# Kernel tuning notes

Measured on AMD Instinct MI355X. Metric: run time of the kernel, lower is better.

## Reference

```python
import jax, jax.numpy as jnp
import numpy as np

N, E, D = 50000, 800000, 128
H, C = 8, 16  # heads, hidden_per_head; H*C == D
NEG_SLOPE = 0.15


def setup_inputs() -> dict:
    key = jax.random.key(0)
    ks = jax.random.split(key, 8)
    x = jax.random.normal(ks[0], (N, D), dtype=jnp.float32)
    edge_index = jax.random.randint(ks[1], (2, E), 0, N, dtype=jnp.int32)
    s = 1.0 / np.sqrt(D)
    return {
        "x": x,
        "edge_index": edge_index,
        "ln_g": jnp.ones((D,), jnp.float32),
        "ln_b": jnp.zeros((D,), jnp.float32),
        "W_l": jax.random.normal(ks[2], (D, H * C), jnp.float32) * s,
        "b_l": jnp.zeros((H * C,), jnp.float32),
        "W_r": jax.random.normal(ks[3], (D, H * C), jnp.float32) * s,
        "b_r": jnp.zeros((H * C,), jnp.float32),
        "att": jax.random.normal(ks[4], (H, C), jnp.float32) * (1.0 / np.sqrt(C)),
        "bias": jnp.zeros((H * C,), jnp.float32),
    }


def _layernorm(x, g, b, eps=1e-5):
    mu = jnp.mean(x, axis=-1, keepdims=True)
    var = jnp.mean(jnp.square(x - mu), axis=-1, keepdims=True)
    return (x - mu) * jax.lax.rsqrt(var + eps) * g + b


def reference(x, edge_index, ln_g, ln_b, W_l, b_l, W_r, b_r, att, bias):
    src, dst = edge_index[0], edge_index[1]
    h = _layernorm(x, ln_g, ln_b)                      # [N, D]
    xl = (h @ W_l + b_l).reshape(N, H, C)              # source-side transform
    xr = (h @ W_r + b_r).reshape(N, H, C)              # target-side transform
    # GATv2 edge attention: leaky_relu(x_j + x_i) . att
    e = xl[src] + xr[dst]                              # [E, H, C]
    e_act = jnp.where(e > 0, e, NEG_SLOPE * e)
    alpha = jnp.einsum('ehc,hc->eh', e_act, att)       # [E, H]
    # segment softmax over edges grouped by destination node
    m = jax.ops.segment_max(alpha, dst, num_segments=N)   # [N, H]
    ex = jnp.exp(alpha - m[dst])                           # [E, H]
    denom = jax.ops.segment_sum(ex, dst, num_segments=N)  # [N, H]
    a = ex / (denom[dst] + 1e-16)                          # [E, H]
    # weighted message aggregation (scatter-add)
    msg = xl[src] * a[:, :, None]                          # [E, H, C]
    out = jax.ops.segment_sum(msg, dst, num_segments=N)   # [N, H, C]
    out = out.reshape(N, H * C) + bias
    h2 = jax.nn.relu(out)                                  # act='relu', dropout off (eval)
    return x + h2                                          # proj is Identity (in_dim == out_dim)
```

## Files before the change

### kernel.cpp

```cpp
#include <hip/hip_runtime.h>

typedef unsigned int uint32;
typedef __attribute__((ext_vector_type(4))) float f32x4;
typedef __attribute__((ext_vector_type(2))) float f32x2;
typedef __attribute__((ext_vector_type(8))) short bf16x8;
typedef __attribute__((ext_vector_type(4))) uint32 u32x4;

#define NEG_SLOPE 0.15f
#define GPB 2

__device__ __forceinline__ float2 bf2_to_f2(uint32 u) {
  union { uint32 i; float f; } a, b;
  a.i = u << 16;
  b.i = u & 0xffff0000u;
  return make_float2(a.f, b.f);
}

__device__ __forceinline__ f32x2 unpk(uint32 u) {
  union { uint32 i; float f; } lo, hi;
  lo.i = u << 16; hi.i = u & 0xffff0000u;
  f32x2 r; r.x = lo.f; r.y = hi.f; return r;
}

__device__ __forceinline__ float bf_to_f(unsigned short s) {
  union { uint32 i; float f; } u;
  u.i = ((uint32)s) << 16;
  return u.f;
}

__device__ __forceinline__ unsigned short f32_to_bf16(float f) {
  union { float f; uint32 i; } u; u.f = f;
  uint32 r = u.i + 0x7fffu + ((u.i >> 16) & 1u);
  return (unsigned short)(r >> 16);
}

__device__ __forceinline__ uint32 pack_bf2(float x, float y) {
  return (uint32)f32_to_bf16(x) | ((uint32)f32_to_bf16(y) << 16);
}

__device__ __forceinline__ float2 loadpair(const void* p, size_t i, int isbf) {
  if (isbf) return bf2_to_f2(((const uint32*)p)[i]);
  return ((const float2*)p)[i];
}

__device__ __forceinline__ float2 loadpair_nt(const void* p, size_t i, int isbf) {
  if (isbf) {
    uint32 u = __builtin_nontemporal_load((const uint32*)p + i);
    return bf2_to_f2(u);
  }
  f32x2 v = __builtin_nontemporal_load((const f32x2*)p + i);
  return make_float2(v.x, v.y);
}

__device__ __forceinline__ float loadelem(const void* p, size_t i, int isbf) {
  if (isbf) return bf_to_f(((const unsigned short*)p)[i]);
  return ((const float*)p)[i];
}

__device__ __forceinline__ int get_isbf(const void* ln_g) {
  return ((const uint32*)ln_g)[0] != 0x3F800000u ? 1 : 0;
}

__device__ __forceinline__ float dpp_swap1(float x) {
  union { float f; int i; } u, r;
  u.f = x;
  r.i = __builtin_amdgcn_mov_dpp(u.i, 0xB1, 0xF, 0xF, false);
  return r.f;
}

__device__ __forceinline__ f32x2 pk_add(f32x2 a, f32x2 b) {
  f32x2 d;
  asm("v_pk_add_f32 %0, %1, %2" : "=v"(d) : "v"(a), "v"(b));
  return d;
}
__device__ __forceinline__ f32x2 pk_mul(f32x2 a, f32x2 b) {
  f32x2 d;
  asm("v_pk_mul_f32 %0, %1, %2" : "=v"(d) : "v"(a), "v"(b));
  return d;
}
__device__ __forceinline__ f32x2 pk_fma(f32x2 a, f32x2 b, f32x2 c) {
  f32x2 d;
  asm("v_pk_fma_f32 %0, %1, %2, %3" : "=v"(d) : "v"(a), "v"(b), "v"(c));
  return d;
}
__device__ __forceinline__ float exp2_raw(float x) {
  float r;
  asm("v_exp_f32 %0, %1" : "=v"(r) : "v"(x));
  return r;
}

__global__ __launch_bounds__(256) void prep_hist_k(
    const void* __restrict__ Wl, const void* __restrict__ Wr,
    const void* __restrict__ bl, const void* __restrict__ br,
    const void* __restrict__ att, const void* __restrict__ obias,
    const void* __restrict__ ln_g, const void* __restrict__ ln_b,
    unsigned short* __restrict__ Wt, float* __restrict__ c1,
    float* __restrict__ c2b, float* __restrict__ att_c,
    float* __restrict__ obias_c,
    const int* __restrict__ ei, int* __restrict__ cntg,
    int E, int Eb, int R)
{
  int b = blockIdx.x;
  if (b < 128) {
    int isbf = get_isbf(ln_g);
    int id = b * 256 + threadIdx.x;
    int n = id >> 7, k = id & 127;
    float g = loadelem(ln_g, k, isbf);
    float v = (n < 128) ? loadelem(Wl, (size_t)k * 128 + n, isbf)
                        : loadelem(Wr, (size_t)k * 128 + (n - 128), isbf);
    Wt[(size_t)n * 128 + k] = f32_to_bf16(g * v);
    if (id < 128) {
      att_c[id]   = loadelem(att, id, isbf) * 1.44269504088896f;
      obias_c[id] = loadelem(obias, id, isbf);
    }
  } else if (b < 192) {
    int isbf = get_isbf(ln_g);
    int w = threadIdx.x >> 6, lane = threadIdx.x & 63;
    int n = (b - 128) * 4 + w;
    const void* W = (n < 128) ? Wl : Wr;
    int nn = n & 127;
    float s1 = 0.f, s2 = 0.f;
    #pragma unroll
    for (int t = 0; t < 2; ++t) {
      int kk = t * 64 + lane;
      float wv = loadelem(W, (size_t)kk * 128 + nn, isbf);
      s1 += loadelem(ln_g, kk, isbf) * wv;
      s2 += loadelem(ln_b, kk, isbf) * wv;
    }
    #pragma unroll
    for (int off = 1; off < 64; off <<= 1) {
      s1 += __shfl_xor(s1, off, 64);
      s2 += __shfl_xor(s2, off, 64);
    }
    if (lane == 0) {
      c1[n] = s1;
      c2b[n] = s2 + ((n < 128) ? loadelem(bl, nn, isbf) : loadelem(br, nn, isbf));
    }
  } else {
    __shared__ int hist[256];
    int hb = b - 192, tid = threadIdx.x;
    hist[tid] = 0;
    __syncthreads();
    int startE = hb * Eb, endE = min(E, startE + Eb);
    const int* dp = ei + E;
    int nfull = (endE > startE) ? ((endE - startE) >> 2) : 0;
    for (int g = tid; g < nfull; g += 256) {
      int4 d = *(const int4*)(dp + startE + g * 4);
      atomicAdd(&hist[((uint32)d.x) >> 8], 1);
      atomicAdd(&hist[((uint32)d.y) >> 8], 1);
      atomicAdd(&hist[((uint32)d.z) >> 8], 1);
      atomicAdd(&hist[((uint32)d.w) >> 8], 1);
    }
    int rem0 = startE + nfull * 4;
    if (rem0 + tid < endE) atomicAdd(&hist[((uint32)dp[rem0 + tid]) >> 8], 1);
    __syncthreads();
    if (tid < R) cntg[tid * 256 + hb] = hist[tid];
  }
}

__global__ __launch_bounds__(1024) void scanA_k(const int* __restrict__ in,
    int* __restrict__ outl, int* __restrict__ psum, int n)
{
  __shared__ int wsum[16];
  int tid = threadIdx.x, lane = tid & 63, w = tid >> 6;
  int i = blockIdx.x * 1024 + tid;
  int v = (i < n) ? in[i] : 0;
  int xs = v;
  #pragma unroll
  for (int off = 1; off < 64; off <<= 1) {
    int y = __shfl_up(xs, off, 64);
    if (lane >= off) xs += y;
  }
  if (lane == 63) wsum[w] = xs;
  __syncthreads();
  if (w == 0) {
    int sv = (lane < 16) ? wsum[lane] : 0;
    int ss = sv;
    #pragma unroll
    for (int off = 1; off < 16; off <<= 1) {
      int y = __shfl_up(ss, off, 64);
      if (lane >= off) ss += y;
    }
    if (lane < 16) wsum[lane] = ss - sv;
    if (lane == 15) psum[blockIdx.x] = ss;
  }
  __syncthreads();
  if (i < n) outl[i] = wsum[w] + xs - v;
}

__device__ __forceinline__ void load_group(bf16x8* slot, const void* x,
                                           int isbf, int rl, int quad) {
  if (isbf) {
    const unsigned short* xp = (const unsigned short*)x + (size_t)rl * 128 + quad * 8;
    #pragma unroll
    for (int kc = 0; kc < 4; ++kc) slot[kc] = *(const bf16x8*)(xp + kc * 32);
  } else {
    const float* xp = (const float*)x + (size_t)rl * 128 + quad * 8;
    #pragma unroll
    for (int kc = 0; kc < 4; ++kc) {
      float4 a0 = *(const float4*)(xp + kc * 32);
      float4 a1 = *(const float4*)(xp + kc * 32 + 4);
      union { bf16x8 v; uint32 u[4]; } av;
      av.u[0] = pack_bf2(a0.x, a0.y);
      av.u[1] = pack_bf2(a0.z, a0.w);
      av.u[2] = pack_bf2(a1.x, a1.y);
      av.u[3] = pack_bf2(a1.z, a1.w);
      slot[kc] = av.v;
    }
  }
}

__global__ __launch_bounds__(256) void bin_gemm_k(
    const int* __restrict__ ei, const int* __restrict__ cbase,
    const int* __restrict__ psum, uint32* __restrict__ binned,
    int E, int Eb, int R, int nbScan,
    const void* __restrict__ x, const void* __restrict__ ln_g,
    const unsigned short* __restrict__ Wt,
    const float* __restrict__ c1, const float* __restrict__ c2b,
    unsigned short* __restrict__ xl, unsigned short* __restrict__ xr,
    int nrows)
{
  if (blockIdx.x < 256) {
    __shared__ int cur[256];
    __shared__ int spsum[64];
    int b = blockIdx.x, tid = threadIdx.x;
    if (tid < 64) {
      int v = (tid < nbScan) ? psum[tid] : 0;
      int xs = v;
      #pragma unroll
      for (int off = 1; off < 64; off <<= 1) {
        int y = __shfl_up(xs, off, 64);
        if (tid >= off) xs += y;
      }
      spsum[tid] = xs - v;
    }
    __syncthreads();
    if (tid < R) {
      int idx = tid * 256 + b;
      cur[tid] = cbase[idx] + spsum[idx >> 10];
    }
    __syncthreads();
    int startE = b * Eb, endE = min(E, startE + Eb);
    int nfull = (endE > startE) ? ((endE - startE) >> 2) : 0;
    for (int g = tid; g < nfull; g += 256) {
      int e = startE + g * 4;
      int4 s = *(const int4*)(ei + e);
      int4 d = *(const int4*)(ei + E + e);
      int p0 = atomicAdd(&cur[((uint32)d.x) >> 8], 1);
      binned[p0] = (uint32)s.x | (((uint32)d.x & 255u) << 16);
      int p1 = atomicAdd(&cur[((uint32)d.y) >> 8], 1);
      binned[p1] = (uint32)s.y | (((uint32)d.y & 255u) << 16);
      int p2 = atomicAdd(&cur[((uint32)d.z) >> 8], 1);
      binned[p2] = (uint32)s.z | (((uint32)d.z & 255u) << 16);
      int p3 = atomicAdd(&cur[((uint32)d.w) >> 8], 1);
      binned[p3] = (uint32)s.w | (((uint32)d.w & 255u) << 16);
    }
    int rem0 = startE + nfull * 4;
    if (rem0 + tid < endE) {
      int e = rem0 + tid;
      uint32 src = (uint32)ei[e], dst = (uint32)ei[E + e];
      int pos = atomicAdd(&cur[dst >> 8], 1);
      binned[pos] = src | ((dst & 255u) << 16);
    }
    return;
  }

  int bid  = blockIdx.x - 256;
  int isbf = get_isbf(ln_g);
  int lane = threadIdx.x & 63;
  int w    = threadIdx.x >> 6;
  int m16  = lane & 15;
  int quad = lane >> 4;
  int base = bid * (GPB * 16);

  bf16x8 araw[GPB][4];
  #pragma unroll
  for (int g2 = 0; g2 < GPB; ++g2) {
    int r = base + g2 * 16 + m16;
    if (r >= nrows) r = nrows - 1;
    load_group(araw[g2], x, isbf, r, quad);
  }

  bf16x8 bfrag[4][4];
  #pragma unroll
  for (int nt = 0; nt < 4; ++nt)
    #pragma unroll
    for (int kc = 0; kc < 4; ++kc)
      bfrag[nt][kc] = *(const bf16x8*)(
          Wt + (size_t)(w * 64 + nt * 16 + m16) * 128 + kc * 32 + quad * 8);

  float c1v[4], c2v[4];
  #pragma unroll
  for (int nt = 0; nt < 4; ++nt) {
    int col = w * 64 + nt * 16 + m16;
    c1v[nt] = c1[col];
    c2v[nt] = c2b[col];
  }

  unsigned short* dst = (w < 2) ? xl : xr;
  int cb = (w & 1) * 64;

  #pragma unroll
  for (int g2 = 0; g2 < GPB; ++g2) {
    bf16x8* A = araw[g2];

    float s = 0.f, s2 = 0.f;
    #pragma unroll
    for (int kc = 0; kc < 4; ++kc) {
      union { bf16x8 v; uint32 u[4]; } uu; uu.v = A[kc];
      #pragma unroll
      for (int j = 0; j < 4; ++j) {
        float2 t = bf2_to_f2(uu.u[j]);
        s += t.x + t.y;
        s2 += t.x * t.x + t.y * t.y;
      }
    }
    s  += __shfl_xor(s, 16, 64);  s2 += __shfl_xor(s2, 16, 64);
    s  += __shfl_xor(s, 32, 64);  s2 += __shfl_xor(s2, 32, 64);
    float mu  = s * (1.0f / 128.0f);
    float var = fmaxf(s2 * (1.0f / 128.0f) - mu * mu, 0.0f);
    float rs  = rsqrtf(var + 1e-5f);
    float rm  = rs * mu;

    f32x4 acc[4];
    #pragma unroll
    for (int nt = 0; nt < 4; ++nt) acc[nt] = (f32x4){0.f, 0.f, 0.f, 0.f};
    #pragma unroll
    for (int kc = 0; kc < 4; ++kc)
      #pragma unroll
      for (int nt = 0; nt < 4; ++nt)
        acc[nt] = __builtin_amdgcn_mfma_f32_16x16x32_bf16(A[kc], bfrag[nt][kc], acc[nt], 0, 0, 0);

    float rs_j[4], rm_j[4];
    #pragma unroll
    for (int j = 0; j < 4; ++j) {
      rs_j[j] = __shfl(rs, quad * 4 + j, 64);
      rm_j[j] = __shfl(rm, quad * 4 + j, 64);
    }

    #pragma unroll
    for (int nt = 0; nt < 4; ++nt) {
      #pragma unroll
      for (int j = 0; j < 4; ++j) {
        int r = base + g2 * 16 + quad * 4 + j;
        if (r < nrows)
          dst[(size_t)r * 128 + cb + nt * 16 + m16] =
              f32_to_bf16(rs_j[j] * acc[nt][j] - rm_j[j] * c1v[nt] + c2v[nt]);
      }
    }
  }
}

__global__ __launch_bounds__(1024) void rangesort_k(
    const uint32* __restrict__ binned, const int* __restrict__ cbase,
    const int* __restrict__ psum,
    int* __restrict__ starts, unsigned short* __restrict__ csr16,
    int E, int N, int R, int nbScan)
{
  __shared__ int hist[256];
  __shared__ int wsum[4];
  __shared__ int cur[256];
  __shared__ int spsum[64];
  int r = blockIdx.x;
  int tid = threadIdx.x, lane = tid & 63, w = tid >> 6;

  if (tid < 64) {
    int pv = (tid < nbScan) ? psum[tid] : 0;
    int pxs = pv;
    #pragma unroll
    for (int off = 1; off < 64; off <<= 1) {
      int y = __shfl_up(pxs, off, 64);
      if (tid >= off) pxs += y;
    }
    spsum[tid] = pxs - pv;
  }
  if (tid < 256) hist[tid] = 0;
  __syncthreads();

  int i0 = r * 256;
  int segStart = cbase[i0] + spsum[i0 >> 10];
  int segEnd;
  if (r + 1 < R) {
    int i1 = (r + 1) * 256;
    segEnd = cbase[i1] + spsum[i1 >> 10];
  } else {
    segEnd = E;
  }
  if (r == 0) {
    if (tid == 0) starts[N] = E;
    if (tid < 32) csr16[E + tid] = 0;
  }

  for (int i = segStart + tid; i < segEnd; i += 1024)
    atomicAdd(&hist[(binned[i] >> 16) & 255u], 1);
  __syncthreads();

  int v = 0, xs = 0;
  if (tid < 256) {
    v = hist[tid];
    xs = v;
    #pragma unroll
    for (int off = 1; off < 64; off <<= 1) {
      int y = __shfl_up(xs, off, 64);
      if (lane >= off) xs += y;
    }
    if (lane == 63) wsum[w] = xs;
  }
  __syncthreads();
  if (tid < 256) {
    int woff = 0;
    #pragma unroll
    for (int i = 0; i < 4; ++i) if (i < w) woff += wsum[i];
    int st = segStart + woff + xs - v;
    int node = (r << 8) + tid;
    if (node < N) starts[node] = st;
    cur[tid] = st;
  }
  __syncthreads();

  for (int i = segStart + tid; i < segEnd; i += 1024) {
    uint32 pk = binned[i];
    int d = (pk >> 16) & 255u;
    int pos = atomicAdd(&cur[d], 1);
    csr16[pos] = (unsigned short)(pk & 0xffffu);
  }
}

__global__ __launch_bounds__(256) void agg_k(
    const uint32* __restrict__ xl32,
    const uint32* __restrict__ xr32,
    const int* __restrict__ starts, const unsigned short* __restrict__ csr16,
    const void* __restrict__ x, const void* __restrict__ ln_g,
    const float* __restrict__ att_c, const float* __restrict__ obias_c,
    void* __restrict__ out, int n)
{
  int node = blockIdx.x * 4 + (threadIdx.x >> 6);
  if (node >= n) return;
  int isbf = get_isbf(ln_g);
  int lane = threadIdx.x & 63;
  int q    = lane >> 4;
  int sub  = lane & 15;

  u32x4 xru = __builtin_nontemporal_load(
      (const u32x4*)(xr32 + (size_t)node * 64 + sub * 4));
  f32x2 xr0 = unpk(xru.x), xr1 = unpk(xru.y), xr2 = unpk(xru.z), xr3 = unpk(xru.w);
  const f32x2* atp = (const f32x2*)(att_c + sub * 8);
  f32x2 t0 = atp[0], t1 = atp[1], t2 = atp[2], t3 = atp[3];
  f32x2 ns; ns.x = NEG_SLOPE; ns.y = NEG_SLOPE;

  float lsum = 0.f;
  f32x2 ac[4];
  #pragma unroll
  for (int i = 0; i < 4; ++i) { ac[i].x = 0.f; ac[i].y = 0.f; }

  int p0 = __builtin_amdgcn_readfirstlane(starts[node]);
  int p1 = __builtin_amdgcn_readfirstlane(starts[node + 1]);

#define AGG_BODY(XU, OK) do { \
    f32x2 a0 = unpk((XU).x), a1 = unpk((XU).y), a2 = unpk((XU).z), a3 = unpk((XU).w); \
    f32x2 e0 = pk_add(a0, xr0), e1 = pk_add(a1, xr1); \
    f32x2 e2 = pk_add(a2, xr2), e3 = pk_add(a3, xr3); \
    f32x2 m0 = pk_mul(e0, ns), m1 = pk_mul(e1, ns); \
    f32x2 m2 = pk_mul(e2, ns), m3 = pk_mul(e3, ns); \
    e0.x = fmaxf(e0.x, m0.x); e0.y = fmaxf(e0.y, m0.y); \
    e1.x = fmaxf(e1.x, m1.x); e1.y = fmaxf(e1.y, m1.y); \
    e2.x = fmaxf(e2.x, m2.x); e2.y = fmaxf(e2.y, m2.y); \
    e3.x = fmaxf(e3.x, m3.x); e3.y = fmaxf(e3.y, m3.y); \
    f32x2 dt = pk_mul(e0, t0); \
    dt = pk_fma(e1, t1, dt); \
    dt = pk_fma(e2, t2, dt); \
    dt = pk_fma(e3, t3, dt); \
    float dot = dt.x + dt.y; \
    dot += dpp_swap1(dot); \
    float pw = (OK) ? exp2_raw(dot) : 0.f; \
    lsum += pw; \
    f32x2 pw2; pw2.x = pw; pw2.y = pw; \
    ac[0] = pk_fma(pw2, a0, ac[0]); \
    ac[1] = pk_fma(pw2, a1, ac[1]); \
    ac[2] = pk_fma(pw2, a2, ac[2]); \
    ac[3] = pk_fma(pw2, a3, ac[3]); \
  } while (0)

  if (p0 < p1) {
    uint32 so = (uint32)(sub * 4);
    const unsigned short* csp = csr16 + p0 + q;
    uint32 j0 = csp[0];
    uint32 j1 = csp[4];
    uint32 j2 = csp[8];
    uint32 j3 = csp[12];
    uint4 xu0 = *(const uint4*)(xl32 + (size_t)(j0 * 64u + so));
    uint4 xu1 = *(const uint4*)(xl32 + (size_t)(j1 * 64u + so));
    int pq   = p0 + q;
    int p1m4 = p1 - 4;
    for (int p = p0; p < p1; p += 8) {
      uint4 xA = xu0;
      xu0 = *(const uint4*)(xl32 + (size_t)(j2 * 64u + so));
      j2  = csp[16];
      AGG_BODY(xA, pq < p1);
      uint4 xB = xu1;
      xu1 = *(const uint4*)(xl32 + (size_t)(j3 * 64u + so));
      j3  = csp[20];
      AGG_BODY(xB, pq < p1m4);
      csp += 8;
      pq  += 8;
    }
  }
#undef AGG_BODY

  lsum += __shfl_xor(lsum, 16, 64);
  lsum += __shfl_xor(lsum, 32, 64);
  #pragma unroll
  for (int i = 0; i < 4; ++i) {
    ac[i].x += __shfl_xor(ac[i].x, 16, 64);
    ac[i].x += __shfl_xor(ac[i].x, 32, 64);
    ac[i].y += __shfl_xor(ac[i].y, 16, 64);
    ac[i].y += __shfl_xor(ac[i].y, 32, 64);
  }

  if (q == 0) {
    float inv = 1.0f / (lsum + 1e-16f);
    float4 b0 = *(const float4*)(obias_c + sub * 8);
    float4 b1 = *(const float4*)(obias_c + sub * 8 + 4);
    float2 rx[4];
    #pragma unroll
    for (int i = 0; i < 4; ++i)
      rx[i] = loadpair_nt(x, (size_t)node * 64 + sub * 4 + i, isbf);
    float o0 = rx[0].x + fmaxf(ac[0].x * inv + b0.x, 0.f);
    float o1 = rx[0].y + fmaxf(ac[0].y * inv + b0.y, 0.f);
    float o2 = rx[1].x + fmaxf(ac[1].x * inv + b0.z, 0.f);
    float o3 = rx[1].y + fmaxf(ac[1].y * inv + b0.w, 0.f);
    float o4 = rx[2].x + fmaxf(ac[2].x * inv + b1.x, 0.f);
    float o5 = rx[2].y + fmaxf(ac[2].y * inv + b1.y, 0.f);
    float o6 = rx[3].x + fmaxf(ac[3].x * inv + b1.z, 0.f);
    float o7 = rx[3].y + fmaxf(ac[3].y * inv + b1.w, 0.f);
    if (isbf) {
      u32x4 ov;
      ov.x = pack_bf2(o0, o1); ov.y = pack_bf2(o2, o3);
      ov.z = pack_bf2(o4, o5); ov.w = pack_bf2(o6, o7);
      __builtin_nontemporal_store(ov, (u32x4*)((uint32*)out + (size_t)node * 64 + sub * 4));
    } else {
      f32x4 f0; f0.x = o0; f0.y = o1; f0.z = o2; f0.w = o3;
      f32x4 f1; f1.x = o4; f1.y = o5; f1.z = o6; f1.w = o7;
      __builtin_nontemporal_store(f0, (f32x4*)((float*)out + (size_t)node * 128 + sub * 8));
      __builtin_nontemporal_store(f1, (f32x4*)((float*)out + (size_t)node * 128 + sub * 8 + 4));
    }
  }
}

static inline char* align16(char* p) {
  return (char*)(((uintptr_t)p + 15) & ~(uintptr_t)15);
}

extern "C" void kernel_launch(void* const* d_in, const int* in_sizes, int n_in,
                              void* d_out, int out_size, void* d_ws, size_t ws_size,
                              hipStream_t stream) {
  const void* x    = d_in[0];
  const int*  ei   = (const int*)d_in[1];
  const void* ln_g = d_in[2];
  const void* ln_b = d_in[3];
  const void* Wl   = d_in[4];
  const void* bl   = d_in[5];
  const void* Wr   = d_in[6];
  const void* br   = d_in[7];
  const void* att  = d_in[8];
  const void* bias = d_in[9];

  int N = in_sizes[0] / 128;
  int E = in_sizes[1] / 2;
  int R = (N + 255) >> 8;
  int L = R * 256;
  int Eb = (((E + 255) / 256) + 3) & ~3;

  char* ws = (char*)d_ws;
  unsigned short* xl = (unsigned short*)ws; ws = align16(ws + (size_t)N * 128 * 2);
  unsigned short* xr = (unsigned short*)ws; ws = align16(ws + (size_t)N * 128 * 2);
  unsigned short* Wt = (unsigned short*)ws; ws = align16(ws + 256 * 128 * 2);
  float* c1      = (float*)ws;              ws = align16(ws + 256 * 4);
  float* c2b     = (float*)ws;              ws = align16(ws + 256 * 4);
  float* att_c   = (float*)ws;              ws = align16(ws + 128 * 4);
  float* obias_c = (float*)ws;              ws = align16(ws + 128 * 4);
  int* cntg      = (int*)ws;                ws = align16(ws + (size_t)L * 4);
  int* cbase     = (int*)ws;                ws = align16(ws + (size_t)L * 4);
  int* psum      = (int*)ws;                ws = align16(ws + 64 * 4);
  int* starts    = (int*)ws;                ws = align16(ws + (size_t)(N + 1) * 4);
  uint32* binned = (uint32*)ws;             ws = align16(ws + (size_t)E * 4);
  unsigned short* csr16 = (unsigned short*)ws; ws = align16(ws + (size_t)(E + 32) * 2);

  int nbScan = (L + 1023) / 1024;
  int nGemmB = (N + GPB * 16 - 1) / (GPB * 16);

  hipLaunchKernelGGL(prep_hist_k, dim3(448), dim3(256), 0, stream,
                     Wl, Wr, bl, br, att, bias, ln_g, ln_b,
                     Wt, c1, c2b, att_c, obias_c,
                     ei, cntg, E, Eb, R);
  hipLaunchKernelGGL(scanA_k, dim3(nbScan), dim3(1024), 0, stream, cntg, cbase, psum, L);
  hipLaunchKernelGGL(bin_gemm_k, dim3(256 + nGemmB), dim3(256), 0, stream,
                     ei, cbase, psum, binned, E, Eb, R, nbScan,
                     x, ln_g, Wt, c1, c2b, xl, xr, N);
  hipLaunchKernelGGL(rangesort_k, dim3(R), dim3(1024), 0, stream,
                     binned, cbase, psum, starts, csr16, E, N, R, nbScan);
  hipLaunchKernelGGL(agg_k, dim3((N + 3) / 4), dim3(256), 0, stream,
                     (const uint32*)xl, (const uint32*)xr, starts, csr16,
                     x, ln_g, att_c, obias_c, d_out, N);
}
```

Measured before the change: 174.0 us.

## Stage binning and range-sort scatters in LDS before coalesced global writes

The binning blocks now do their local counting sort into a shared-memory buffer first, using per-block bucket counts prefix-scanned in-block. They then write the sorted run to global memory with mostly contiguous stores, replacing scattered atomic-indexed global writes. The range-sort kernel likewise scatters into an LDS array and copies it out contiguously. Both paths fall back to the old global scatter when segments exceed the LDS capacity. The larger shared-memory footprint can reduce occupancy, and the binning kernel shares launch slots with the GEMM blocks.

```diff
diff --git a/kernel.cpp b/kernel.cpp
--- a/kernel.cpp
+++ b/kernel.cpp
@@ -8,6 +8,8 @@
 
 #define NEG_SLOPE 0.15f
 #define GPB 2
+#define SBUF_MAX 4096
+#define CSR_MAX  6144
 
 __device__ __forceinline__ float2 bf2_to_f2(uint32 u) {
   union { uint32 i; float f; } a, b;
@@ -211,7 +213,8 @@
 }
 
 __global__ __launch_bounds__(256) void bin_gemm_k(
-    const int* __restrict__ ei, const int* __restrict__ cbase,
+    const int* __restrict__ ei, const int* __restrict__ cntg,
+    const int* __restrict__ cbase,
     const int* __restrict__ psum, uint32* __restrict__ binned,
     int E, int Eb, int R, int nbScan,
     const void* __restrict__ x, const void* __restrict__ ln_g,
@@ -221,9 +224,15 @@
     int nrows)
 {
   if (blockIdx.x < 256) {
+    __shared__ int spsum[64];
+    __shared__ int wsum2[4];
+    __shared__ int lofs[256];
+    __shared__ int gbase[256];
     __shared__ int cur[256];
-    __shared__ int spsum[64];
+    __shared__ uint32 sbuf[SBUF_MAX];
     int b = blockIdx.x, tid = threadIdx.x;
+    int lane = tid & 63, w = tid >> 6;
+
     if (tid < 64) {
       int v = (tid < nbScan) ? psum[tid] : 0;
       int xs = v;
@@ -234,33 +243,51 @@
       }
       spsum[tid] = xs - v;
     }
+    int v2 = (tid < R) ? cntg[tid * 256 + b] : 0;
+    int xs2 = v2;
+    #pragma unroll
+    for (int off = 1; off < 64; off <<= 1) {
+      int y = __shfl_up(xs2, off, 64);
+      if (lane >= off) xs2 += y;
+    }
+    if (lane == 63) wsum2[w] = xs2;
     __syncthreads();
+
+    int woff2 = 0;
+    #pragma unroll
+    for (int i = 0; i < 4; ++i) if (i < w) woff2 += wsum2[i];
+    int lo = woff2 + xs2 - v2;
+    lofs[tid] = lo;
+    int startE = b * Eb, endE = min(E, startE + Eb);
     if (tid < R) {
       int idx = tid * 256 + b;
-      cur[tid] = cbase[idx] + spsum[idx >> 10];
-    }
-    __syncthreads();
-    int startE = b * Eb, endE = min(E, startE + Eb);
-    int nfull = (endE > startE) ? ((endE - startE) >> 2) : 0;
-    for (int g = tid; g < nfull; g += 256) {
-      int e = startE + g * 4;
-      int4 s = *(const int4*)(ei + e);
-      int4 d = *(const int4*)(ei + E + e);
-      int p0 = atomicAdd(&cur[((uint32)d.x) >> 8], 1);
-      binned[p0] = (uint32)s.x | (((uint32)d.x & 255u) << 16);
-      int p1 = atomicAdd(&cur[((uint32)d.y) >> 8], 1);
-      binned[p1] = (uint32)s.y | (((uint32)d.y & 255u) << 16);
-      int p2 = atomicAdd(&cur[((uint32)d.z) >> 8], 1);
-      binned[p2] = (uint32)s.z | (((uint32)d.z & 255u) << 16);
-      int p3 = atomicAdd(&cur[((uint32)d.w) >> 8], 1);
-      binned[p3] = (uint32)s.w | (((uint32)d.w & 255u) << 16);
-    }
-    int rem0 = startE + nfull * 4;
-    if (rem0 + tid < endE) {
-      int e = rem0 + tid;
-      uint32 src = (uint32)ei[e], dst = (uint32)ei[E + e];
-      int pos = atomicAdd(&cur[dst >> 8], 1);
-      binned[pos] = src | ((dst & 255u) << 16);
+      gbase[tid] = cbase[idx] + spsum[idx >> 10];
+    }
+
+    if (Eb <= SBUF_MAX) {
+      cur[tid] = lo;
+      __syncthreads();
+      for (int e = startE + tid; e < endE; e += 256) {
+        uint32 src = (uint32)ei[e], dst = (uint32)ei[E + e];
+        uint32 r = dst >> 8;
+        int pos = atomicAdd(&cur[r], 1);
+        sbuf[pos] = src | ((dst & 255u) << 16) | (r << 24);
+      }
+      __syncthreads();
+      int nloc = endE - startE;
+      for (int i = tid; i < nloc; i += 256) {
+        uint32 e2 = sbuf[i];
+        uint32 r = e2 >> 24;
+        binned[gbase[r] + (i - lofs[r])] = e2 & 0x00FFFFFFu;
+      }
+    } else {
+      cur[tid] = (tid < R) ? gbase[tid] : 0;
+      __syncthreads();
+      for (int e = startE + tid; e < endE; e += 256) {
+        uint32 src = (uint32)ei[e], dst = (uint32)ei[E + e];
+        int pos = atomicAdd(&cur[dst >> 8], 1);
+        binned[pos] = src | ((dst & 255u) << 16);
+      }
     }
     return;
   }
@@ -361,6 +388,7 @@
   __shared__ int wsum[4];
   __shared__ int cur[256];
   __shared__ int spsum[64];
+  __shared__ unsigned short csr_l[CSR_MAX];
   int r = blockIdx.x;
   int tid = threadIdx.x, lane = tid & 63, w = tid >> 6;
 
@@ -386,6 +414,8 @@
   } else {
     segEnd = E;
   }
+  int segLen = segEnd - segStart;
+  bool lds_ok = (segLen <= CSR_MAX);
   if (r == 0) {
     if (tid == 0) starts[N] = E;
     if (tid < 32) csr16[E + tid] = 0;
@@ -411,18 +441,30 @@
     int woff = 0;
     #pragma unroll
     for (int i = 0; i < 4; ++i) if (i < w) woff += wsum[i];
-    int st = segStart + woff + xs - v;
+    int st_local = woff + xs - v;
     int node = (r << 8) + tid;
-    if (node < N) starts[node] = st;
-    cur[tid] = st;
+    if (node < N) starts[node] = segStart + st_local;
+    cur[tid] = lds_ok ? st_local : segStart + st_local;
   }
   __syncthreads();
 
-  for (int i = segStart + tid; i < segEnd; i += 1024) {
-    uint32 pk = binned[i];
-    int d = (pk >> 16) & 255u;
-    int pos = atomicAdd(&cur[d], 1);
-    csr16[pos] = (unsigned short)(pk & 0xffffu);
+  if (lds_ok) {
+    for (int i = segStart + tid; i < segEnd; i += 1024) {
+      uint32 pk = binned[i];
+      int d = (pk >> 16) & 255u;
+      int pos = atomicAdd(&cur[d], 1);
+      csr_l[pos] = (unsigned short)(pk & 0xffffu);
+    }
+    __syncthreads();
+    for (int i = tid; i < segLen; i += 1024)
+      csr16[segStart + i] = csr_l[i];
+  } else {
+    for (int i = segStart + tid; i < segEnd; i += 1024) {
+      uint32 pk = binned[i];
+      int d = (pk >> 16) & 255u;
+      int pos = atomicAdd(&cur[d], 1);
+      csr16[pos] = (unsigned short)(pk & 0xffffu);
+    }
   }
 }
 
@@ -595,7 +637,7 @@
                      ei, cntg, E, Eb, R);
   hipLaunchKernelGGL(scanA_k, dim3(nbScan), dim3(1024), 0, stream, cntg, cbase, psum, L);
   hipLaunchKernelGGL(bin_gemm_k, dim3(256 + nGemmB), dim3(256), 0, stream,
-                     ei, cbase, psum, binned, E, Eb, R, nbScan,
+                     ei, cntg, cbase, psum, binned, E, Eb, R, nbScan,
                      x, ln_g, Wt, c1, c2b, xl, xr, N);
   hipLaunchKernelGGL(rangesort_k, dim3(R), dim3(1024), 0, stream,
                      binned, cbase, psum, starts, csr16, E, N, R, nbScan);
```

Measured after the change: 170.8 us. No clear change (-1.8%).
